# Performance work log

Measured on AMD Instinct MI355X. Metric: run time of the kernel, lower is better.

Reference implementation:

```python
import jax, jax.numpy as jnp
import numpy as np

N_NODES = 50000
N_EDGES = 1600000
IN_CH = 128
HEADS = 4
OUT_PER_HEAD = 32  # out_channels // heads with concat=True
NEG_SLOPE = 0.2    # GATConv default leaky_relu slope
SOFTMAX_EPS = 1e-16  # PyG scatter-softmax denominator eps
LN_EPS = 1e-5


def setup_inputs() -> dict:
    key = jax.random.key(0)
    ks = jax.random.split(key, 8)
    x = jax.random.normal(ks[0], (N_NODES, IN_CH), dtype=jnp.float32)
    edge_index = jax.random.randint(ks[1], (2, N_EDGES), 0, N_NODES, dtype=jnp.int32)
    W = jax.random.normal(ks[2], (IN_CH, HEADS * OUT_PER_HEAD), dtype=jnp.float32) * (1.0 / np.sqrt(IN_CH))
    att_src = jax.random.normal(ks[3], (HEADS, OUT_PER_HEAD), dtype=jnp.float32) * 0.1
    att_dst = jax.random.normal(ks[4], (HEADS, OUT_PER_HEAD), dtype=jnp.float32) * 0.1
    bias = jnp.zeros((HEADS * OUT_PER_HEAD,), dtype=jnp.float32)
    gamma = jnp.ones((HEADS * OUT_PER_HEAD,), dtype=jnp.float32)
    beta = jnp.zeros((HEADS * OUT_PER_HEAD,), dtype=jnp.float32)
    return {"x": x, "edge_index": edge_index, "W": W, "att_src": att_src,
            "att_dst": att_dst, "bias": bias, "gamma": gamma, "beta": beta}


def reference(x, edge_index, W, att_src, att_dst, bias, gamma, beta):
    N = x.shape[0]
    H, C = att_src.shape
    # GATConv default add_self_loops=True
    loop = jnp.arange(N, dtype=edge_index.dtype)
    src = jnp.concatenate([edge_index[0], loop])  # message source j
    dst = jnp.concatenate([edge_index[1], loop])  # aggregation target i

    h = (x @ W).reshape(N, H, C)                      # [N,H,C]
    a_s = jnp.einsum('nhc,hc->nh', h, att_src)        # [N,H]
    a_d = jnp.einsum('nhc,hc->nh', h, att_dst)        # [N,H]

    logits = jax.nn.leaky_relu(a_s[src] + a_d[dst], NEG_SLOPE)  # [E,H]
    # segment softmax over edges grouped by destination node
    m = jax.ops.segment_max(logits, dst, num_segments=N)        # [N,H]
    m = jnp.where(jnp.isfinite(m), m, 0.0)
    e = jnp.exp(logits - m[dst])
    s = jax.ops.segment_sum(e, dst, num_segments=N)             # [N,H]
    alpha = e / (s[dst] + SOFTMAX_EPS)                          # [E,H]

    msg = h[src] * alpha[:, :, None]                            # [E,H,C]
    out = jax.ops.segment_sum(msg, dst, num_segments=N)         # [N,H,C]
    out = out.reshape(N, H * C) + bias

    mu = out.mean(axis=-1, keepdims=True)
    var = ((out - mu) ** 2).mean(axis=-1, keepdims=True)
    y = (out - mu) / jnp.sqrt(var + LN_EPS) * gamma + beta
    return jax.nn.elu(y)
```

## Files before the change

### kernel.cpp

```cpp
#include <hip/hip_runtime.h>
#include <hip/hip_bf16.h>

typedef __hip_bfloat16 bf16;
typedef unsigned int u32;
typedef unsigned short u16;
typedef __attribute__((ext_vector_type(8))) short bf16x8;
typedef __attribute__((ext_vector_type(4))) float f32x4;

constexpr int N   = 50000;
constexpr int E   = 1600000;
constexpr int C   = 128;
constexpr int H   = 4;
constexpr int NB  = 782;
constexpr int CAP = 2560;
constexpr int NCH = 256;
constexpr int CHUNK = E / NCH;
constexpr int GEMM_BLOCKS = 782;
constexpr float NEG  = 0.2f;
constexpr float SEPS = 1e-16f;
constexpr float LEPS = 1e-5f;

__device__ __forceinline__ float lo16(u32 v) { return __uint_as_float(v << 16); }
__device__ __forceinline__ float hi16(u32 v) { return __uint_as_float(v & 0xFFFF0000u); }
__device__ __forceinline__ u16 bfbits(float f) {
    __hip_bfloat16 h = __float2bfloat16(f);
    return *reinterpret_cast<u16*>(&h);
}

__global__ __launch_bounds__(256) void k0_wprep(
    const float* __restrict__ W, u16* __restrict__ wt_hi, u16* __restrict__ wt_lo)
{
    const int i = blockIdx.x * 256 + threadIdx.x;
    const int c = i >> 7, k = i & 127;
    const float w = W[k * 128 + c];
    const __hip_bfloat16 h = __float2bfloat16(w);
    const float fh = __bfloat162float(h);
    wt_hi[i] = *(const u16*)&h;
    wt_lo[i] = bfbits(w - fh);
}

__global__ __launch_bounds__(256, 4) void f1_gemm_count(
    const float* __restrict__ x,
    const u16* __restrict__ wt_hi, const u16* __restrict__ wt_lo,
    const float* __restrict__ att_s, const float* __restrict__ att_d,
    const int* __restrict__ ei,
    u16* __restrict__ hb, float* __restrict__ as_, float* __restrict__ ad_,
    u32* __restrict__ gcnt)
{
    __shared__ u32 lcnt[NB];
    const int t = threadIdx.x;

    if (blockIdx.x >= GEMM_BLOCKS) {
        const int c = blockIdx.x - GEMM_BLOCKS;
        const int base = c * CHUNK;
        for (int i = t; i < NB; i += 256) lcnt[i] = 0;
        __syncthreads();
        for (int i = t; i < CHUNK; i += 256)
            atomicAdd(&lcnt[((u32)ei[E + base + i]) >> 6], 1u);
        __syncthreads();
        for (int i = t; i < NB; i += 256) gcnt[i * NCH + c] = lcnt[i];
        return;
    }

    const int m0   = blockIdx.x * 64;
    const int lane = t & 63;
    const int w    = t >> 6;
    const int bcol = lane & 15;
    const int akg  = lane >> 4;
    const int aq   = akg;

    const int arow = min(m0 + w * 16 + bcol, N - 1);
    const float* xr = x + (size_t)arow * 128;

    f32x4 acc[8];
#pragma unroll
    for (int nt = 0; nt < 8; ++nt) acc[nt] = f32x4{0.f, 0.f, 0.f, 0.f};

#pragma unroll
    for (int ks = 0; ks < 4; ++ks) {
        const float4 q0 = *(const float4*)(xr + ks * 32 + akg * 8);
        const float4 q1 = *(const float4*)(xr + ks * 32 + akg * 8 + 4);
        const float f[8] = {q0.x, q0.y, q0.z, q0.w, q1.x, q1.y, q1.z, q1.w};
        bf16x8 Ah, Al;
#pragma unroll
        for (int j = 0; j < 8; ++j) {
            const __hip_bfloat16 hh = __float2bfloat16(f[j]);
            Ah[j] = *(const short*)&hh;
            const __hip_bfloat16 hl = __float2bfloat16(f[j] - __bfloat162float(hh));
            Al[j] = *(const short*)&hl;
        }
        const u16* bpk = wt_hi + bcol * 128 + ks * 32 + akg * 8;
        const u16* bqk = wt_lo + bcol * 128 + ks * 32 + akg * 8;
#pragma unroll
        for (int nt = 0; nt < 8; ++nt) {
            const bf16x8 Bh = *(const bf16x8*)(bpk + nt * 2048);
            const bf16x8 Bl = *(const bf16x8*)(bqk + nt * 2048);
            acc[nt] = __builtin_amdgcn_mfma_f32_16x16x32_bf16(Ah, Bh, acc[nt], 0, 0, 0);
            acc[nt] = __builtin_amdgcn_mfma_f32_16x16x32_bf16(Al, Bh, acc[nt], 0, 0, 0);
            acc[nt] = __builtin_amdgcn_mfma_f32_16x16x32_bf16(Ah, Bl, acc[nt], 0, 0, 0);
        }
    }

#pragma unroll
    for (int nt = 0; nt < 8; ++nt) {
        const int ch = nt * 16 + bcol;
#pragma unroll
        for (int r = 0; r < 4; ++r) {
            const int node = m0 + w * 16 + aq * 4 + r;
            if (node < N) hb[(size_t)node * 128 + ch] = bfbits(acc[nt][r]);
        }
    }

    float ps[4][4], pd[4][4];
#pragma unroll
    for (int h = 0; h < 4; ++h) {
        const float a0 = att_s[32 * h + bcol], a1 = att_s[32 * h + 16 + bcol];
        const float d0 = att_d[32 * h + bcol], d1 = att_d[32 * h + 16 + bcol];
#pragma unroll
        for (int r = 0; r < 4; ++r) {
            ps[h][r] = acc[2 * h][r] * a0 + acc[2 * h + 1][r] * a1;
            pd[h][r] = acc[2 * h][r] * d0 + acc[2 * h + 1][r] * d1;
        }
    }
#pragma unroll
    for (int off = 1; off < 16; off <<= 1) {
#pragma unroll
        for (int h = 0; h < 4; ++h)
#pragma unroll
            for (int r = 0; r < 4; ++r) {
                ps[h][r] += __shfl_xor(ps[h][r], off, 64);
                pd[h][r] += __shfl_xor(pd[h][r], off, 64);
            }
    }
    if (bcol == 0) {
#pragma unroll
        for (int r = 0; r < 4; ++r) {
            const int node = m0 + w * 16 + aq * 4 + r;
            if (node < N) {
#pragma unroll
                for (int h = 0; h < 4; ++h) {
                    as_[node * H + h] = ps[h][r];
                    ad_[node * H + h] = pd[h][r];
                }
            }
        }
    }
}

__global__ __launch_bounds__(256) void s2a_scan(
    const u32* __restrict__ gcnt, u32* __restrict__ gbase, u32* __restrict__ tot)
{
    __shared__ u32 wsum[4];
    const int b = blockIdx.x, t = threadIdx.x, lane = t & 63, w = t >> 6;
    const u32 v = gcnt[b * NCH + t];
    u32 incl = v;
#pragma unroll
    for (int off = 1; off < 64; off <<= 1) {
        u32 u = __shfl_up(incl, off, 64);
        if (lane >= off) incl += u;
    }
    if (lane == 63) wsum[w] = incl;
    __syncthreads();
    u32 wpre = 0;
#pragma unroll
    for (int i = 0; i < 4; ++i) if (i < w) wpre += wsum[i];
    gbase[b * NCH + t] = wpre + incl - v;
    if (t == 255) tot[b] = wpre + incl;
}

__global__ __launch_bounds__(256) void kbinB(
    const int* __restrict__ ei, const u32* __restrict__ gbase,
    const u32* __restrict__ tot, u32* __restrict__ pairs)
{
    __shared__ u32 sl[NB];
    __shared__ u32 lfill[NB];
    __shared__ u32 wsum[4];
    const int t = threadIdx.x, lane = t & 63, w = t >> 6;
    const int c = blockIdx.x;

    u32 carry = 0;
    for (int q = 0; q < 4; ++q) {
        const int idx = q * 256 + t;
        const u32 v = (idx < NB) ? tot[idx] : 0u;
        u32 incl = v;
#pragma unroll
        for (int off = 1; off < 64; off <<= 1) {
            u32 u = __shfl_up(incl, off, 64);
            if (lane >= off) incl += u;
        }
        if (lane == 63) wsum[w] = incl;
        __syncthreads();
        u32 wpre = 0, wtot = 0;
#pragma unroll
        for (int i = 0; i < 4; ++i) { const u32 s = wsum[i]; wtot += s; if (i < w) wpre += s; }
        if (idx < NB) sl[idx] = carry + wpre + (incl - v) + gbase[(size_t)idx * NCH + c];
        carry += wtot;
        __syncthreads();
    }
    for (int i = t; i < NB; i += 256) lfill[i] = 0u;
    __syncthreads();

    const int base = c * CHUNK;
    for (int i = t; i < CHUNK; i += 256) {
        const u32 src = (u32)ei[base + i];
        const u32 dst = (u32)ei[E + base + i];
        const u32 b = dst >> 6;
        const u32 pos = atomicAdd(&lfill[b], 1u);
        pairs[sl[b] + pos] = src | ((dst & 63u) << 16);
    }
}

__global__ __launch_bounds__(256) void kfill2(
    const u32* __restrict__ pairs, const u32* __restrict__ tot,
    int* __restrict__ row_ptr, u16* __restrict__ col)
{
    __shared__ u32 spr[CAP];
    __shared__ u16 scol[CAP];
    __shared__ int jcnt[64], joff[64], jcur[64];
    __shared__ u32 rsum[4];
    const int b = blockIdx.x, t = threadIdx.x;
    const int lane = t & 63, w = t >> 6;

    u32 part = 0;
    for (int i = t; i < b; i += 256) part += tot[i];
#pragma unroll
    for (int off = 32; off; off >>= 1) part += __shfl_xor(part, off, 64);
    if (lane == 0) rsum[w] = part;
    if (t < 64) jcnt[t] = 0;
    __syncthreads();
    const int base = (int)(rsum[0] + rsum[1] + rsum[2] + rsum[3]);
    const int cntb = (int)tot[b];

    const u32* pr = pairs + base;
    for (int i = t; i < cntb; i += 256) spr[i] = pr[i];
    __syncthreads();
    for (int i = t; i < cntb; i += 256) atomicAdd(&jcnt[spr[i] >> 16], 1);
    __syncthreads();
    if (t < 64) {
        int v = jcnt[t], incl = v;
#pragma unroll
        for (int off = 1; off < 64; off <<= 1) {
            int u = __shfl_up(incl, off, 64);
            if (t >= off) incl += u;
        }
        joff[t] = incl - v;
        const int n = b * 64 + t;
        if (n < N) row_ptr[n] = base + joff[t];
        jcur[t] = 0;
    }
    __syncthreads();
    for (int i = t; i < cntb; i += 256) {
        const u32 p = spr[i];
        const int j = p >> 16;
        const int pos = atomicAdd(&jcur[j], 1);
        scol[joff[j] + pos] = (u16)(p & 0xFFFFu);
    }
    __syncthreads();
    for (int i = t; i < cntb; i += 256) col[base + i] = scol[i];
    if (b == 0 && t == 0) row_ptr[N] = E;
}

__global__ __launch_bounds__(256) void kd_agg_ln(
    const int* __restrict__ row_ptr, const u16* __restrict__ col,
    const u32* __restrict__ hb, const float* __restrict__ as_,
    const float* __restrict__ ad_,
    const float* __restrict__ bias, const float* __restrict__ gamma,
    const float* __restrict__ beta, float* __restrict__ out, int n0)
{
    __shared__ float wlds[4][64];
    const int tid  = threadIdx.x;
    const int lane = tid & 63;
    const int wv   = __builtin_amdgcn_readfirstlane(tid >> 6);
    const int n    = __builtin_amdgcn_readfirstlane(n0 + (int)blockIdx.x * 4 + (tid >> 6));
    if (n >= N) return;

    const int head  = lane >> 4;
    const int eoff  = lane & 15;
    const int wbase = head << 4;
    float* __restrict__ wrow = wlds[wv];

    const float adn = ad_[n * H + head];
    const float asn = as_[n * H + head];

    float ls = asn + adn;
    ls = fmaxf(ls, NEG * ls);
    const float wself = __expf(ls);
    float den = (eoff == 0) ? wself : 0.f;
    const u32 hvs = hb[n * 64 + lane];
    float num0 = wself * lo16(hvs);
    float num1 = wself * hi16(hvs);

    const int k0  = row_ptr[n];
    const int deg = row_ptr[n + 1] - k0;
    const int ntiles = (deg + 15) >> 4;

    const int cnt0 = deg < 16 ? deg : 16;
    const int cnt1 = (deg - 16) < 16 ? (deg - 16) : 16;
    int colv_cur = (eoff < cnt0) ? (int)col[k0 + eoff]      : 0;
    int colv_nxt = (eoff < cnt1) ? (int)col[k0 + 16 + eoff] : 0;
    float a_cur  = as_[colv_cur * H + head];
    int cntc = cnt0, cntn = cnt1;

    int k = k0;
    for (int t = 0; t < ntiles; ++t, k += 16) {
        const int rem2 = deg - 16 * (t + 2);
        const int cnt2 = rem2 < 16 ? rem2 : 16;
        const int cf_raw = (int)col[k + 32 + eoff];
        const int colv_f = (eoff < cnt2) ? cf_raw : 0;

        float le = a_cur + adn;
        le = fmaxf(le, NEG * le);
        const float w = (eoff < cntc) ? __expf(le) : 0.f;
        den += w;
        wrow[lane] = w;
        const int colc = colv_cur;

#define GL(i) const u32* rp##i = hb + ((size_t)(u32)__builtin_amdgcn_readlane(colc, i) << 6); \
              const u32 v##i = rp##i[lane];
        GL(0) GL(1) GL(2) GL(3) GL(4) GL(5) GL(6) GL(7)
        GL(8) GL(9) GL(10) GL(11) GL(12) GL(13) GL(14) GL(15)
#undef GL
        __builtin_amdgcn_sched_barrier(0);

        const float a_n = as_[colv_nxt * H + head];
        __builtin_amdgcn_sched_barrier(0);

        {
            const float4 wa = *(const float4*)(wrow + wbase + 0);
            num0 = fmaf(wa.x, lo16(v0), num0);  num1 = fmaf(wa.x, hi16(v0), num1);
            num0 = fmaf(wa.y, lo16(v1), num0);  num1 = fmaf(wa.y, hi16(v1), num1);
            num0 = fmaf(wa.z, lo16(v2), num0);  num1 = fmaf(wa.z, hi16(v2), num1);
            num0 = fmaf(wa.w, lo16(v3), num0);  num1 = fmaf(wa.w, hi16(v3), num1);
            const float4 wb = *(const float4*)(wrow + wbase + 4);
            num0 = fmaf(wb.x, lo16(v4), num0);  num1 = fmaf(wb.x, hi16(v4), num1);
            num0 = fmaf(wb.y, lo16(v5), num0);  num1 = fmaf(wb.y, hi16(v5), num1);
            num0 = fmaf(wb.z, lo16(v6), num0);  num1 = fmaf(wb.z, hi16(v6), num1);
            num0 = fmaf(wb.w, lo16(v7), num0);  num1 = fmaf(wb.w, hi16(v7), num1);
            const float4 wc = *(const float4*)(wrow + wbase + 8);
            num0 = fmaf(wc.x, lo16(v8), num0);  num1 = fmaf(wc.x, hi16(v8), num1);
            num0 = fmaf(wc.y, lo16(v9), num0);  num1 = fmaf(wc.y, hi16(v9), num1);
            num0 = fmaf(wc.z, lo16(v10), num0); num1 = fmaf(wc.z, hi16(v10), num1);
            num0 = fmaf(wc.w, lo16(v11), num0); num1 = fmaf(wc.w, hi16(v11), num1);
            const float4 wd = *(const float4*)(wrow + wbase + 12);
            num0 = fmaf(wd.x, lo16(v12), num0); num1 = fmaf(wd.x, hi16(v12), num1);
            num0 = fmaf(wd.y, lo16(v13), num0); num1 = fmaf(wd.y, hi16(v13), num1);
            num0 = fmaf(wd.z, lo16(v14), num0); num1 = fmaf(wd.z, hi16(v14), num1);
            num0 = fmaf(wd.w, lo16(v15), num0); num1 = fmaf(wd.w, hi16(v15), num1);
        }

        colv_cur = colv_nxt; colv_nxt = colv_f;
        a_cur = a_n;
        cntc = cntn; cntn = cnt2;
    }

#pragma unroll
    for (int off = 1; off < 16; off <<= 1) den += __shfl_xor(den, off, 64);

    const int c0 = lane * 2;
    const float inv_den = 1.f / (den + SEPS);
    const float2 bi = *(const float2*)(bias + c0);
    float v0 = num0 * inv_den + bi.x;
    float v1 = num1 * inv_den + bi.y;

    float sum = v0 + v1;
#pragma unroll
    for (int off = 32; off; off >>= 1) sum += __shfl_xor(sum, off, 64);
    const float mu = sum * (1.0f / C);
    const float d0 = v0 - mu, d1 = v1 - mu;
    float sq = d0 * d0 + d1 * d1;
#pragma unroll
    for (int off = 32; off; off >>= 1) sq += __shfl_xor(sq, off, 64);
    const float inv = rsqrtf(sq * (1.0f / C) + LEPS);
    const float2 ga = *(const float2*)(gamma + c0);
    const float2 be = *(const float2*)(beta  + c0);
    float y0 = d0 * inv * ga.x + be.x;
    float y1 = d1 * inv * ga.y + be.y;
    y0 = y0 > 0.f ? y0 : __expf(y0) - 1.f;
    y1 = y1 > 0.f ? y1 : __expf(y1) - 1.f;
    float2 o; o.x = y0; o.y = y1;
    *(float2*)(out + (size_t)n * C + c0) = o;
}

extern "C" void kernel_launch(void* const* d_in, const int* in_sizes, int n_in,
                              void* d_out, int out_size, void* d_ws, size_t ws_size,
                              hipStream_t stream)
{
    const float* x     = (const float*)d_in[0];
    const int*   ei    = (const int*)  d_in[1];
    const float* W     = (const float*)d_in[2];
    const float* att_s = (const float*)d_in[3];
    const float* att_d = (const float*)d_in[4];
    const float* bias  = (const float*)d_in[5];
    const float* gamma = (const float*)d_in[6];
    const float* beta  = (const float*)d_in[7];
    float* out = (float*)d_out;

    char* p = (char*)d_ws;
    bf16*  hb      = (bf16*)p;   p += (size_t)N * C * sizeof(bf16);
    float* as_     = (float*)p;  p += (size_t)N * H * sizeof(float);
    float* ad_     = (float*)p;  p += (size_t)N * H * sizeof(float);
    u32*   pairs   = (u32*)p;    p += (size_t)E * sizeof(u32);
    u16*   col     = (u16*)p;    p += ((size_t)(E + 64) * sizeof(u16) + 15) & ~(size_t)15;
    int*   row_ptr = (int*)p;    p += ((size_t)(N + 1) * sizeof(int) + 15) & ~(size_t)15;
    u32*   gcnt    = (u32*)p;    p += (size_t)NB * NCH * sizeof(u32);
    u32*   gbase   = (u32*)p;    p += (size_t)NB * NCH * sizeof(u32);
    u32*   tot     = (u32*)p;    p += (((size_t)NB * sizeof(u32)) + 15) & ~(size_t)15;
    u16*   wt_hi   = (u16*)p;    p += (size_t)128 * 128 * sizeof(u16);
    u16*   wt_lo   = (u16*)p;

    k0_wprep<<<64, 256, 0, stream>>>(W, wt_hi, wt_lo);
    f1_gemm_count<<<GEMM_BLOCKS + NCH, 256, 0, stream>>>(
        x, wt_hi, wt_lo, att_s, att_d, ei, (u16*)hb, as_, ad_, gcnt);
    s2a_scan<<<NB, 256, 0, stream>>>(gcnt, gbase, tot);
    kbinB<<<NCH, 256, 0, stream>>>(ei, gbase, tot, pairs);
    kfill2<<<NB, 256, 0, stream>>>(pairs, tot, row_ptr, col);
    kd_agg_ln<<<(25000 * 64) / 256, 256, 0, stream>>>(
        row_ptr, col, (const u32*)hb, as_, ad_, bias, gamma, beta, out, 0);
    kd_agg_ln<<<(25000 * 64) / 256, 256, 0, stream>>>(
        row_ptr, col, (const u32*)hb, as_, ad_, bias, gamma, beta, out, 25000);
}
```

Baseline: 225.4 us.

## Fold attention vectors into GEMM weights and hoist bin-base scan into one kernel

Precomputes W·att_src and W·att_dst as eight extra weight columns, so the GEMM produces the attention logits directly through a ninth MFMA tile. This replaces the per-lane dot products and shuffle reductions. The edge-count pass is split out of the fused GEMM kernel, and the GEMM is launched as two halves. A new single-wave scan computes the bucket base offsets once, instead of every kbinB and kfill2 block redoing that prefix sum. In exchange there are more kernel launches, and the folded weights are rounded to split bf16, which may slightly change logit precision.

```diff
diff --git a/kernel.cpp b/kernel.cpp
--- a/kernel.cpp
+++ b/kernel.cpp
@@ -15,7 +15,7 @@
 constexpr int CAP = 2560;
 constexpr int NCH = 256;
 constexpr int CHUNK = E / NCH;
-constexpr int GEMM_BLOCKS = 782;
+constexpr int WT_COLS = 144;
 constexpr float NEG  = 0.2f;
 constexpr float SEPS = 1e-16f;
 constexpr float LEPS = 1e-5f;
@@ -28,41 +28,40 @@
 }
 
 __global__ __launch_bounds__(256) void k0_wprep(
-    const float* __restrict__ W, u16* __restrict__ wt_hi, u16* __restrict__ wt_lo)
+    const float* __restrict__ W,
+    const float* __restrict__ att_s, const float* __restrict__ att_d,
+    u16* __restrict__ wt_hi, u16* __restrict__ wt_lo)
 {
     const int i = blockIdx.x * 256 + threadIdx.x;
+    if (i >= WT_COLS * 128) return;
     const int c = i >> 7, k = i & 127;
-    const float w = W[k * 128 + c];
+    float w = 0.f;
+    if (c < 128) {
+        w = W[k * 128 + c];
+    } else if (c < 136) {
+        const int vc = c - 128;
+        const int h = vc & 3;
+        const float* att = (vc < 4) ? att_s : att_d;
+        float s = 0.f;
+#pragma unroll
+        for (int j = 0; j < 32; ++j)
+            s = fmaf(W[k * 128 + h * 32 + j], att[h * 32 + j], s);
+        w = s;
+    }
     const __hip_bfloat16 h = __float2bfloat16(w);
     const float fh = __bfloat162float(h);
     wt_hi[i] = *(const u16*)&h;
     wt_lo[i] = bfbits(w - fh);
 }
 
-__global__ __launch_bounds__(256, 4) void f1_gemm_count(
+__global__ __launch_bounds__(256, 4) void kg_gemm(
     const float* __restrict__ x,
     const u16* __restrict__ wt_hi, const u16* __restrict__ wt_lo,
-    const float* __restrict__ att_s, const float* __restrict__ att_d,
-    const int* __restrict__ ei,
     u16* __restrict__ hb, float* __restrict__ as_, float* __restrict__ ad_,
-    u32* __restrict__ gcnt)
-{
-    __shared__ u32 lcnt[NB];
-    const int t = threadIdx.x;
-
-    if (blockIdx.x >= GEMM_BLOCKS) {
-        const int c = blockIdx.x - GEMM_BLOCKS;
-        const int base = c * CHUNK;
-        for (int i = t; i < NB; i += 256) lcnt[i] = 0;
-        __syncthreads();
-        for (int i = t; i < CHUNK; i += 256)
-            atomicAdd(&lcnt[((u32)ei[E + base + i]) >> 6], 1u);
-        __syncthreads();
-        for (int i = t; i < NB; i += 256) gcnt[i * NCH + c] = lcnt[i];
-        return;
-    }
-
-    const int m0   = blockIdx.x * 64;
+    int mb)
+{
+    const int t    = threadIdx.x;
+    const int m0   = (mb + (int)blockIdx.x) * 64;
     const int lane = t & 63;
     const int w    = t >> 6;
     const int bcol = lane & 15;
@@ -72,27 +71,26 @@
     const int arow = min(m0 + w * 16 + bcol, N - 1);
     const float* xr = x + (size_t)arow * 128;
 
-    f32x4 acc[8];
-#pragma unroll
-    for (int nt = 0; nt < 8; ++nt) acc[nt] = f32x4{0.f, 0.f, 0.f, 0.f};
+    f32x4 acc[9];
+#pragma unroll
+    for (int nt = 0; nt < 9; ++nt) acc[nt] = f32x4{0.f, 0.f, 0.f, 0.f};
 
 #pragma unroll
     for (int ks = 0; ks < 4; ++ks) {
         const float4 q0 = *(const float4*)(xr + ks * 32 + akg * 8);
         const float4 q1 = *(const float4*)(xr + ks * 32 + akg * 8 + 4);
-        const float f[8] = {q0.x, q0.y, q0.z, q0.w, q1.x, q1.y, q1.z, q1.w};
         bf16x8 Ah, Al;
-#pragma unroll
-        for (int j = 0; j < 8; ++j) {
-            const __hip_bfloat16 hh = __float2bfloat16(f[j]);
-            Ah[j] = *(const short*)&hh;
-            const __hip_bfloat16 hl = __float2bfloat16(f[j] - __bfloat162float(hh));
-            Al[j] = *(const short*)&hl;
-        }
+#define CV(idx, val) { const __hip_bfloat16 hh = __float2bfloat16(val); \
+        Ah[idx] = *(const short*)&hh; \
+        const __hip_bfloat16 hl = __float2bfloat16((val) - __bfloat162float(hh)); \
+        Al[idx] = *(const short*)&hl; }
+        CV(0, q0.x) CV(1, q0.y) CV(2, q0.z) CV(3, q0.w)
+        CV(4, q1.x) CV(5, q1.y) CV(6, q1.z) CV(7, q1.w)
+#undef CV
         const u16* bpk = wt_hi + bcol * 128 + ks * 32 + akg * 8;
         const u16* bqk = wt_lo + bcol * 128 + ks * 32 + akg * 8;
 #pragma unroll
-        for (int nt = 0; nt < 8; ++nt) {
+        for (int nt = 0; nt < 9; ++nt) {
             const bf16x8 Bh = *(const bf16x8*)(bpk + nt * 2048);
             const bf16x8 Bl = *(const bf16x8*)(bqk + nt * 2048);
             acc[nt] = __builtin_amdgcn_mfma_f32_16x16x32_bf16(Ah, Bh, acc[nt], 0, 0, 0);
@@ -111,40 +109,29 @@
         }
     }
 
-    float ps[4][4], pd[4][4];
-#pragma unroll
-    for (int h = 0; h < 4; ++h) {
-        const float a0 = att_s[32 * h + bcol], a1 = att_s[32 * h + 16 + bcol];
-        const float d0 = att_d[32 * h + bcol], d1 = att_d[32 * h + 16 + bcol];
-#pragma unroll
-        for (int r = 0; r < 4; ++r) {
-            ps[h][r] = acc[2 * h][r] * a0 + acc[2 * h + 1][r] * a1;
-            pd[h][r] = acc[2 * h][r] * d0 + acc[2 * h + 1][r] * d1;
-        }
-    }
-#pragma unroll
-    for (int off = 1; off < 16; off <<= 1) {
-#pragma unroll
-        for (int h = 0; h < 4; ++h)
-#pragma unroll
-            for (int r = 0; r < 4; ++r) {
-                ps[h][r] += __shfl_xor(ps[h][r], off, 64);
-                pd[h][r] += __shfl_xor(pd[h][r], off, 64);
-            }
-    }
-    if (bcol == 0) {
+    if (bcol < 8) {
+        float* dst = (bcol < 4) ? (as_ + bcol) : (ad_ + (bcol - 4));
 #pragma unroll
         for (int r = 0; r < 4; ++r) {
             const int node = m0 + w * 16 + aq * 4 + r;
-            if (node < N) {
-#pragma unroll
-                for (int h = 0; h < 4; ++h) {
-                    as_[node * H + h] = ps[h][r];
-                    ad_[node * H + h] = pd[h][r];
-                }
-            }
+            if (node < N) dst[(size_t)node * H] = acc[8][r];
         }
     }
+}
+
+__global__ __launch_bounds__(256) void kc_count(
+    const int* __restrict__ ei, u32* __restrict__ gcnt)
+{
+    __shared__ u32 lcnt[NB];
+    const int t = threadIdx.x;
+    const int c = blockIdx.x;
+    const int base = c * CHUNK;
+    for (int i = t; i < NB; i += 256) lcnt[i] = 0;
+    __syncthreads();
+    for (int i = t; i < CHUNK; i += 256)
+        atomicAdd(&lcnt[((u32)ei[E + base + i]) >> 6], 1u);
+    __syncthreads();
+    for (int i = t; i < NB; i += 256) gcnt[i * NCH + c] = lcnt[i];
 }
 
 __global__ __launch_bounds__(256) void s2a_scan(
@@ -168,36 +155,45 @@
     if (t == 255) tot[b] = wpre + incl;
 }
 
+__global__ __launch_bounds__(64) void s2b_scan(
+    const u32* __restrict__ tot, u32* __restrict__ bbase)
+{
+    const int t = threadIdx.x;
+    u32 vals[13];
+    u32 s = 0;
+#pragma unroll
+    for (int i = 0; i < 13; ++i) {
+        int idx = t * 13 + i;
+        u32 v = (idx < NB) ? tot[idx] : 0u;
+        vals[i] = s; s += v;
+    }
+    u32 incl = s;
+#pragma unroll
+    for (int off = 1; off < 64; off <<= 1) {
+        u32 u = __shfl_up(incl, off, 64);
+        if (t >= off) incl += u;
+    }
+    const u32 excl = incl - s;
+#pragma unroll
+    for (int i = 0; i < 13; ++i) {
+        int idx = t * 13 + i;
+        if (idx < NB) bbase[idx] = excl + vals[i];
+    }
+}
+
 __global__ __launch_bounds__(256) void kbinB(
     const int* __restrict__ ei, const u32* __restrict__ gbase,
-    const u32* __restrict__ tot, u32* __restrict__ pairs)
+    const u32* __restrict__ bbase, u32* __restrict__ pairs)
 {
     __shared__ u32 sl[NB];
     __shared__ u32 lfill[NB];
-    __shared__ u32 wsum[4];
-    const int t = threadIdx.x, lane = t & 63, w = t >> 6;
+    const int t = threadIdx.x;
     const int c = blockIdx.x;
 
-    u32 carry = 0;
-    for (int q = 0; q < 4; ++q) {
-        const int idx = q * 256 + t;
-        const u32 v = (idx < NB) ? tot[idx] : 0u;
-        u32 incl = v;
-#pragma unroll
-        for (int off = 1; off < 64; off <<= 1) {
-            u32 u = __shfl_up(incl, off, 64);
-            if (lane >= off) incl += u;
-        }
-        if (lane == 63) wsum[w] = incl;
-        __syncthreads();
-        u32 wpre = 0, wtot = 0;
-#pragma unroll
-        for (int i = 0; i < 4; ++i) { const u32 s = wsum[i]; wtot += s; if (i < w) wpre += s; }
-        if (idx < NB) sl[idx] = carry + wpre + (incl - v) + gbase[(size_t)idx * NCH + c];
-        carry += wtot;
-        __syncthreads();
-    }
-    for (int i = t; i < NB; i += 256) lfill[i] = 0u;
+    for (int i = t; i < NB; i += 256) {
+        sl[i] = bbase[i] + gbase[(size_t)i * NCH + c];
+        lfill[i] = 0u;
+    }
     __syncthreads();
 
     const int base = c * CHUNK;
@@ -212,24 +208,16 @@
 
 __global__ __launch_bounds__(256) void kfill2(
     const u32* __restrict__ pairs, const u32* __restrict__ tot,
-    int* __restrict__ row_ptr, u16* __restrict__ col)
+    const u32* __restrict__ bbase, int* __restrict__ row_ptr, u16* __restrict__ col)
 {
     __shared__ u32 spr[CAP];
     __shared__ u16 scol[CAP];
     __shared__ int jcnt[64], joff[64], jcur[64];
-    __shared__ u32 rsum[4];
     const int b = blockIdx.x, t = threadIdx.x;
-    const int lane = t & 63, w = t >> 6;
-
-    u32 part = 0;
-    for (int i = t; i < b; i += 256) part += tot[i];
-#pragma unroll
-    for (int off = 32; off; off >>= 1) part += __shfl_xor(part, off, 64);
-    if (lane == 0) rsum[w] = part;
+    const int base = (int)bbase[b];
+    const int cntb = (int)tot[b];
     if (t < 64) jcnt[t] = 0;
     __syncthreads();
-    const int base = (int)(rsum[0] + rsum[1] + rsum[2] + rsum[3]);
-    const int cntb = (int)tot[b];
 
     const u32* pr = pairs + base;
     for (int i = t; i < cntb; i += 256) spr[i] = pr[i];
@@ -405,15 +393,18 @@
     u32*   gcnt    = (u32*)p;    p += (size_t)NB * NCH * sizeof(u32);
     u32*   gbase   = (u32*)p;    p += (size_t)NB * NCH * sizeof(u32);
     u32*   tot     = (u32*)p;    p += (((size_t)NB * sizeof(u32)) + 15) & ~(size_t)15;
-    u16*   wt_hi   = (u16*)p;    p += (size_t)128 * 128 * sizeof(u16);
+    u32*   bbase   = (u32*)p;    p += (((size_t)NB * sizeof(u32)) + 15) & ~(size_t)15;
+    u16*   wt_hi   = (u16*)p;    p += (size_t)WT_COLS * 128 * sizeof(u16);
     u16*   wt_lo   = (u16*)p;
 
-    k0_wprep<<<64, 256, 0, stream>>>(W, wt_hi, wt_lo);
-    f1_gemm_count<<<GEMM_BLOCKS + NCH, 256, 0, stream>>>(
-        x, wt_hi, wt_lo, att_s, att_d, ei, (u16*)hb, as_, ad_, gcnt);
+    k0_wprep<<<(WT_COLS * 128 + 255) / 256, 256, 0, stream>>>(W, att_s, att_d, wt_hi, wt_lo);
+    kg_gemm<<<391, 256, 0, stream>>>(x, wt_hi, wt_lo, (u16*)hb, as_, ad_, 0);
+    kg_gemm<<<391, 256, 0, stream>>>(x, wt_hi, wt_lo, (u16*)hb, as_, ad_, 391);
+    kc_count<<<NCH, 256, 0, stream>>>(ei, gcnt);
     s2a_scan<<<NB, 256, 0, stream>>>(gcnt, gbase, tot);
-    kbinB<<<NCH, 256, 0, stream>>>(ei, gbase, tot, pairs);
-    kfill2<<<NB, 256, 0, stream>>>(pairs, tot, row_ptr, col);
+    s2b_scan<<<1, 64, 0, stream>>>(tot, bbase);
+    kbinB<<<NCH, 256, 0, stream>>>(ei, gbase, bbase, pairs);
+    kfill2<<<NB, 256, 0, stream>>>(pairs, tot, bbase, row_ptr, col);
     kd_agg_ln<<<(25000 * 64) / 256, 256, 0, stream>>>(
         row_ptr, col, (const u32*)hb, as_, ad_, bias, gamma, beta, out, 0);
     kd_agg_ln<<<(25000 * 64) / 256, 256, 0, stream>>>(
```

New measurement: 228.5 us. About the same (+1.4%).
